# Kernel optimization log

Hardware: AMD Instinct MI355X
Metric: run time of the kernel (lower is better)

The kernel has to match this reference:

```python
import jax, jax.numpy as jnp
import numpy as np

NUM_HEADS = 16
NUM_GROUPS = 4
EPS = 1e-6


def _rope_tables(seq_len, head_dim):
    inv_freq = 1.0 / (10000.0 ** (jnp.arange(0, head_dim, 2, dtype=jnp.float32) / head_dim))
    t = jnp.arange(seq_len, dtype=jnp.float32)
    freqs = jnp.outer(t, inv_freq)  # [s, hd//2]
    return jnp.sin(freqs), jnp.cos(freqs)


def _apply_rope(x, sin, cos):
    # x: [b, s, h, hd]; sin/cos: [s, hd//2] -> broadcast over batch and heads
    sin = sin[None, :, None, :]
    cos = cos[None, :, None, :]
    x1 = x[..., ::2]
    x2 = x[..., 1::2]
    out1 = x1 * cos - x2 * sin
    out2 = x1 * sin + x2 * cos
    return jnp.stack([out1, out2], axis=-1).reshape(x.shape).astype(x.dtype)


def _rmsnorm(x, scale):
    var = jnp.mean(jnp.square(x), axis=-1, keepdims=True)
    return x * jax.lax.rsqrt(var + EPS) * scale


def setup_inputs() -> dict:
    key = jax.random.key(0)
    b, s, d = 16, 512, 2048
    hd = d // NUM_HEADS
    g = NUM_GROUPS
    ks = jax.random.split(key, 9)
    std = 0.02
    return {
        "x": jax.random.normal(ks[0], (b, s, d), dtype=jnp.float32),
        "Wq": jax.random.normal(ks[1], (d, d), dtype=jnp.float32) * std,
        "bq": jnp.zeros((d,), dtype=jnp.float32),
        "Wk": jax.random.normal(ks[2], (d, g * hd), dtype=jnp.float32) * std,
        "bk": jnp.zeros((g * hd,), dtype=jnp.float32),
        "Wv": jax.random.normal(ks[3], (d, g * hd), dtype=jnp.float32) * std,
        "bv": jnp.zeros((g * hd,), dtype=jnp.float32),
        "Wo": jax.random.normal(ks[4], (d, d), dtype=jnp.float32) * std,
        "bo": jnp.zeros((d,), dtype=jnp.float32),
        "q_norm_scale": jnp.ones((hd,), dtype=jnp.float32),
        "k_norm_scale": jnp.ones((hd,), dtype=jnp.float32),
    }


def reference(x, Wq, bq, Wk, bk, Wv, bv, Wo, bo, q_norm_scale, k_norm_scale):
    b, s, d = x.shape
    H, G = NUM_HEADS, NUM_GROUPS
    hd = d // H
    P = H // G  # queries per kv group
    inv_sqrt_hd = hd ** (-0.5)

    q = (x @ Wq + bq).reshape(b, s, H, hd)
    k = (x @ Wk + bk).reshape(b, s, G, hd)
    v = (x @ Wv + bv).reshape(b, s, G, hd)

    q = _rmsnorm(q, q_norm_scale)
    k = _rmsnorm(k, k_norm_scale)

    sin, cos = _rope_tables(s, hd)
    q = _apply_rope(q, sin, cos) * inv_sqrt_hd  # module pre-scales q
    k = _apply_rope(k, sin, cos)

    # GQA attention with causal mask; dot_product_attention applies an
    # additional 1/sqrt(hd) scale on top of the module's pre-scaling.
    qg = q.reshape(b, s, G, P, hd)
    logits = jnp.einsum("bsgph,btgh->bgpst", qg, k) * inv_sqrt_hd
    causal = jnp.tril(jnp.ones((s, s), dtype=bool))
    logits = jnp.where(causal[None, None, None, :, :], logits, jnp.finfo(logits.dtype).min)
    attn = jax.nn.softmax(logits, axis=-1)
    out = jnp.einsum("bgpst,btgh->bsgph", attn, v).reshape(b, s, d)
    return out @ Wo + bo
```

## Files before the change

### kernel.cpp

```cpp
#include <hip/hip_runtime.h>
#include <stdint.h>

typedef __attribute__((ext_vector_type(4))) float floatx4;
typedef __attribute__((ext_vector_type(16))) float floatx16;
typedef __attribute__((ext_vector_type(8))) short short8;

#define BB 16
#define SS 512
#define DD 2048
#define HH_ 16
#define HD 128
#define GG 4
#define MM (BB*SS)
#define NQKV 3072

__device__ __forceinline__ unsigned short f2bf(float f){
  unsigned u = __builtin_bit_cast(unsigned, f);
  u += 0x7fffu + ((u >> 16) & 1u);
  return (unsigned short)(u >> 16);
}
__device__ __forceinline__ float bf2f_lo(unsigned d){
  return __builtin_bit_cast(float, d << 16);
}
__device__ __forceinline__ float bf2f_hi(unsigned d){
  return __builtin_bit_cast(float, d & 0xffff0000u);
}

__device__ __forceinline__ void async_copy16(const void* g, void* l){
  __builtin_amdgcn_global_load_lds((const __attribute__((address_space(1))) unsigned*)g,
                                   (__attribute__((address_space(3))) unsigned*)l,
                                   16, 0, 0);
}

#define PB_CVT   16384
#define PB_TRQ   (PB_CVT + 4096)
#define PB_TRK   (PB_TRQ + 1024)
#define PB_TRV   (PB_TRK + 1024)
#define PB_TRO   (PB_TRV + 4096)
#define PB_ALL   (PB_TRO + 12)

__global__ __launch_bounds__(256) void prep_kernel(
    const float* __restrict__ x,
    const float* __restrict__ Wq, const float* __restrict__ Wk,
    const float* __restrict__ Wv, const float* __restrict__ Wo,
    const float* __restrict__ bq, const float* __restrict__ bk,
    const float* __restrict__ bv,
    unsigned short* __restrict__ xb, unsigned short* __restrict__ WqkvT,
    unsigned short* __restrict__ WoT, float* __restrict__ bqkv)
{
  __shared__ float tile[32][33];
  const int bid = blockIdx.x, tid = threadIdx.x;

  if (bid < PB_CVT) {
    const int i = bid * 256 + tid;
    float4 f = ((const float4*)x)[i];
    ushort4 o;
    o.x = f2bf(f.x); o.y = f2bf(f.y); o.z = f2bf(f.z); o.w = f2bf(f.w);
    ((ushort4*)xb)[i] = o;
    return;
  }
  if (bid < PB_TRO) {
    const float* src; unsigned short* dst; int R, C, b2;
    if (bid < PB_TRQ)      { src = Wq; dst = WqkvT;                          R = 2048; C = 2048; b2 = bid - PB_CVT; }
    else if (bid < PB_TRK) { src = Wk; dst = WqkvT + (size_t)2048 * 2048;    R = 2048; C = 512;  b2 = bid - PB_TRQ; }
    else if (bid < PB_TRV) { src = Wv; dst = WqkvT + (size_t)2560 * 2048;    R = 2048; C = 512;  b2 = bid - PB_TRK; }
    else                   { src = Wo; dst = WoT;                            R = 2048; C = 2048; b2 = bid - PB_TRV; }
    const int nbx = C >> 5;
    const int c0 = (b2 % nbx) * 32, r0 = (b2 / nbx) * 32;
    const int tx = tid & 31, ty = tid >> 5;
    #pragma unroll
    for (int j = 0; j < 32; j += 8)
      tile[ty + j][tx] = src[(size_t)(r0 + ty + j) * C + (c0 + tx)];
    __syncthreads();
    #pragma unroll
    for (int j = 0; j < 32; j += 8)
      dst[(size_t)(c0 + ty + j) * R + (r0 + tx)] = f2bf(tile[tx][ty + j]);
    return;
  }
  {
    const int i = (bid - PB_TRO) * 256 + tid;
    if (i < NQKV)
      bqkv[i] = (i < 2048) ? bq[i] : (i < 2560 ? bk[i - 2048] : bv[i - 2560]);
  }
}

template<bool OUT_BF16>
__global__ __launch_bounds__(512, 2) void gemm256_kernel(
    const unsigned short* __restrict__ A,
    const unsigned short* __restrict__ Bt,
    void* __restrict__ Cout,
    const float* __restrict__ bias,
    int N, int K, int ldc)
{
  __shared__ unsigned short sA[4 * 128 * 64];
  __shared__ unsigned short sB[4 * 128 * 64];

  const int tid  = threadIdx.x;
  const int wave = tid >> 6, lane = tid & 63;
  const int wm = wave >> 2, wn = wave & 3;
  const int l15 = lane & 15, l7 = lane & 7, q4 = lane >> 4;

  const int nbn = N >> 8;
  const int cpx = gridDim.x >> 3;
  const int bid = (blockIdx.x & 7) * cpx + (blockIdx.x >> 3);
  const int m0 = (bid / nbn) * 256;
  const int n0 = (bid % nbn) * 256;

  const int rowOff = wave * 8 + (lane >> 3);
  const int glog   = l7 ^ ((lane >> 3) & 7);
  const unsigned short* gA = A  + (size_t)(m0 + rowOff) * K + glog * 8;
  const unsigned short* gB = Bt + (size_t)(n0 + rowOff) * K + glog * 8;

#define STAGE_A(j, tt) do { \
    unsigned short* d_ = &sA[(2 * ((tt) & 1) + (j)) * 8192 + wave * 512]; \
    const unsigned short* s_ = gA + (size_t)((j) * 128) * K + (tt) * 64; \
    async_copy16(s_, d_); \
    async_copy16(s_ + (size_t)64 * K, d_ + 4096); } while (0)
#define STAGE_B(j, tt) do { \
    unsigned short* d_ = &sB[(2 * ((tt) & 1) + (j)) * 8192 + wave * 512]; \
    const unsigned short* s_ = gB + (size_t)((j) * 128) * K + (tt) * 64; \
    async_copy16(s_, d_); \
    async_copy16(s_ + (size_t)64 * K, d_ + 4096); } while (0)
#define FENCE() asm volatile("" ::: "memory")
#define BAR()   do { FENCE(); __builtin_amdgcn_s_barrier(); FENCE(); } while (0)

  STAGE_B(0, 0); STAGE_B(1, 0); STAGE_A(0, 0); STAGE_A(1, 0);
  STAGE_B(0, 1); STAGE_B(1, 1); STAGE_A(0, 1); STAGE_A(1, 1);

  floatx16 zero16 = {0.f};
  floatx4 acc[8][4];
  #pragma unroll
  for (int i = 0; i < 8; ++i)
    #pragma unroll
    for (int j = 0; j < 4; ++j)
      acc[i][j] = (floatx4){0.f, 0.f, 0.f, 0.f};
  (void)zero16;

  asm volatile("s_waitcnt vmcnt(8)" ::: "memory");
  BAR();

  short8 aF[4][2], bF[4][2];
  const int NT = K >> 6;

  const unsigned short* pA = &sA[l15 * 64];
  const unsigned short* pB = &sB[((wn & 1) * 64 + l15) * 64];
  const int g0 = ((0 + q4) ^ l7) * 8;
  const int g1 = ((4 + q4) ^ l7) * 8;

#define LDA_(fa_, rb_, sa_) do { \
    aF[fa_][0] = *(const short8*)(pA + (sa_) * 8192 + ((rb_) + (fa_) * 16) * 64 + g0); \
    aF[fa_][1] = *(const short8*)(pA + (sa_) * 8192 + ((rb_) + (fa_) * 16) * 64 + g1); } while (0)
#define LDB_(fb_, sb_) do { \
    bF[fb_][0] = *(const short8*)(pB + (sb_) * 8192 + (fb_) * 16 * 64 + g0); \
    bF[fb_][1] = *(const short8*)(pB + (sb_) * 8192 + (fb_) * 16 * 64 + g1); } while (0)
#define MFMA_Q(fa0, fb0) \
    _Pragma("unroll") \
    for (int fa = 0; fa < 4; ++fa) { \
      _Pragma("unroll") \
      for (int fb = 0; fb < 2; ++fb) { \
        acc[(fa0)+fa][(fb0)+fb] = __builtin_amdgcn_mfma_f32_16x16x32_bf16(aF[fa][0], bF[(fb0)+fb][0], acc[(fa0)+fa][(fb0)+fb], 0, 0, 0); \
        acc[(fa0)+fa][(fb0)+fb] = __builtin_amdgcn_mfma_f32_16x16x32_bf16(aF[fa][1], bF[(fb0)+fb][1], acc[(fa0)+fa][(fb0)+fb], 0, 0, 0); \
      } \
    }

  #pragma unroll 1
  for (int t = 0; t < NT; ++t) {
    const int sa = 2 * (t & 1) + wm;
    const int sb = 2 * (t & 1) + (wn >> 1);
    LDB_(0, sb); LDB_(1, sb);
    LDA_(0, 0, sa); LDA_(1, 0, sa); LDA_(2, 0, sa); LDA_(3, 0, sa);
    __builtin_amdgcn_s_setprio(1);
    MFMA_Q(0, 0);
    __builtin_amdgcn_s_setprio(0);
    BAR();
    LDB_(2, sb); LDB_(3, sb);
    __builtin_amdgcn_s_setprio(1);
    MFMA_Q(0, 2);
    __builtin_amdgcn_s_setprio(0);
    BAR();
    LDA_(0, 64, sa); LDA_(1, 64, sa); LDA_(2, 64, sa); LDA_(3, 64, sa);
    if (t + 2 < NT) { STAGE_B(0, t + 2); STAGE_B(1, t + 2); }
    __builtin_amdgcn_s_setprio(1);
    MFMA_Q(4, 0);
    __builtin_amdgcn_s_setprio(0);
    BAR();
    if (t + 2 < NT) {
      STAGE_A(0, t + 2); STAGE_A(1, t + 2);
      asm volatile("s_waitcnt vmcnt(8)" ::: "memory");
    } else if (t + 1 < NT) {
      asm volatile("s_waitcnt vmcnt(0)" ::: "memory");
    }
    __builtin_amdgcn_s_setprio(1);
    MFMA_Q(4, 2);
    __builtin_amdgcn_s_setprio(0);
    BAR();
  }
#undef STAGE_A
#undef STAGE_B
#undef LDA_
#undef LDB_
#undef MFMA_Q
#undef FENCE
#undef BAR

  const int r4 = q4 * 4;
  #pragma unroll
  for (int fb = 0; fb < 4; ++fb) {
    const int col = n0 + wn * 64 + fb * 16 + l15;
    const float bval = bias[col];
    #pragma unroll
    for (int fa = 0; fa < 8; ++fa) {
      const size_t rowb = (size_t)(m0 + wm * 128 + fa * 16 + r4);
      #pragma unroll
      for (int r = 0; r < 4; ++r) {
        const float v = acc[fa][fb][r] + bval;
        if (OUT_BF16)
          ((unsigned short*)Cout)[(rowb + r) * ldc + col] = f2bf(v);
        else
          ((float*)Cout)[(rowb + r) * ldc + col] = v;
      }
    }
  }
}

__global__ __launch_bounds__(256) void norm_vtr_kernel(
    unsigned short* __restrict__ qkv,
    const float* __restrict__ qs, const float* __restrict__ ks,
    unsigned short* __restrict__ vt)
{
  __shared__ unsigned short tileV[32][34];
  const int bid = blockIdx.x, tid = threadIdx.x;

  if (bid < 40960) {
    const int wave = tid >> 6, lane = tid & 63;
    const int gw  = bid * 4 + wave;
    const int row = gw / 20;
    const int hh  = gw % 20;
    const bool isq = hh < 16;

    unsigned* p = (unsigned*)(qkv + (size_t)row * NQKV + hh * 128) + lane;
    unsigned d = *p;
    float x1 = bf2f_lo(d), x2 = bf2f_hi(d);

    float ss = x1 * x1 + x2 * x2;
    #pragma unroll
    for (int off = 32; off; off >>= 1) ss += __shfl_xor(ss, off, 64);
    const float r = rsqrtf(ss * (1.f / 128.f) + 1e-6f);

    const float2 sc = ((const float2*)(isq ? qs : ks))[lane];
    float n1 = x1 * r * sc.x;
    float n2 = x2 * r * sc.y;

    const float t = (float)(row & (SS - 1));
    const float freq = __expf((float)lane * (-2.f / 128.f) * 9.21034037197618f);
    float sn, cs;
    __sincosf(t * freq, &sn, &cs);
    float o1 = n1 * cs - n2 * sn;
    float o2 = n1 * sn + n2 * cs;
    if (isq) { o1 *= (1.f / 128.f); o2 *= (1.f / 128.f); }

    *p = (unsigned)f2bf(o1) | ((unsigned)f2bf(o2) << 16);
    return;
  }
  {
    const int b2 = bid - 40960;
    const int hd0 = (b2 & 3) * 32, t0 = ((b2 >> 2) & 15) * 32, bg = b2 >> 6;
    const int tx = tid & 31, ty = tid >> 5;
    const int b = bg >> 2, g = bg & 3;
    const unsigned short* src = qkv + (size_t)b * SS * NQKV + 2560 + g * HD;
    #pragma unroll
    for (int j = 0; j < 32; j += 8)
      tileV[ty + j][tx] = src[(size_t)(t0 + ty + j) * NQKV + hd0 + tx];
    __syncthreads();
    unsigned short* dst = vt + (size_t)bg * HD * SS;
    #pragma unroll
    for (int j = 0; j < 32; j += 8)
      dst[(size_t)(hd0 + ty + j) * SS + t0 + tx] = tileV[tx][ty + j];
  }
}

__global__ __launch_bounds__(256, 4) void fattn_kernel(
    const unsigned short* __restrict__ qkv,
    const unsigned short* __restrict__ vtb,
    unsigned short* __restrict__ aout)
{
  __shared__ unsigned short sK[64 * 128];
  __shared__ unsigned short sV[128 * 64];
  __shared__ unsigned short sP[4][16 * 64];

  const int lane = threadIdx.x & 63, wave = threadIdx.x >> 6;
  const int quad = lane >> 4, col = lane & 15;
  const int idx = blockIdx.x;
  const int qb = 7 - (idx >> 8);
  const int bh = idx & 255;
  const int b = bh >> 4, h = bh & 15, g = h >> 2;

  const int qrow = qb * 64 + wave * 16 + col;
  const unsigned short* qg = qkv + ((size_t)(b * SS + qrow)) * NQKV + h * HD + quad * 8;
  short8 qf[4];
  #pragma unroll
  for (int c = 0; c < 4; ++c) qf[c] = *(const short8*)(qg + c * 32);

  const unsigned short* kg = qkv + (size_t)b * SS * NQKV + 2048 + g * HD;
  const unsigned short* vg = vtb + ((size_t)(b * GG + g)) * HD * SS;

  floatx4 acc_o[8];
  #pragma unroll
  for (int i = 0; i < 8; ++i) acc_o[i] = (floatx4){0.f, 0.f, 0.f, 0.f};
  float m[4] = {-INFINITY, -INFINITY, -INFINITY, -INFINITY};
  float l[4] = {0.f, 0.f, 0.f, 0.f};

  for (int kt = 0; kt <= qb; ++kt) {
    const int t0 = kt * 64;
    #pragma unroll
    for (int c = 0; c < 4; ++c) {
      const int ci = c * 4 + wave;
      { const int r  = ci * 4 + (lane >> 4);
        const int gl = (lane & 15) ^ (r & 15);
        async_copy16(kg + (size_t)(t0 + r) * NQKV + gl * 8, &sK[ci * 512]); }
      { const int r  = ci * 8 + (lane >> 3);
        const int gl = (lane & 7) ^ (r & 7);
        async_copy16(vg + (size_t)r * SS + t0 + gl * 8, &sV[ci * 512]); }
    }
    __syncthreads();

    floatx4 sc[4];
    #pragma unroll
    for (int s = 0; s < 4; ++s) sc[s] = (floatx4){0.f, 0.f, 0.f, 0.f};
    #pragma unroll
    for (int s = 0; s < 4; ++s) {
      const int trow = s * 16 + col;
      #pragma unroll
      for (int c = 0; c < 4; ++c) {
        const int p = (c * 4 + quad) ^ (trow & 15);
        const short8 kf = *(const short8*)(&sK[trow * 128 + p * 8]);
        sc[s] = __builtin_amdgcn_mfma_f32_16x16x32_bf16(qf[c], kf, sc[s], 0, 0, 0);
      }
    }

    if (kt == qb) {
      #pragma unroll
      for (int s = 0; s < 4; ++s)
        #pragma unroll
        for (int r = 0; r < 4; ++r)
          if (s * 16 + col > wave * 16 + quad * 4 + r) sc[s][r] = -1e30f;
    }

    float mx[4], alpha[4], lsum[4];
    #pragma unroll
    for (int r = 0; r < 4; ++r) {
      mx[r] = fmaxf(fmaxf(sc[0][r], sc[1][r]), fmaxf(sc[2][r], sc[3][r]));
      #pragma unroll
      for (int off = 8; off; off >>= 1) mx[r] = fmaxf(mx[r], __shfl_xor(mx[r], off, 16));
      mx[r] = fmaxf(mx[r], m[r]);
      alpha[r] = __expf(m[r] - mx[r]);
      m[r] = mx[r];
      lsum[r] = 0.f;
    }
    #pragma unroll
    for (int s = 0; s < 4; ++s)
      #pragma unroll
      for (int r = 0; r < 4; ++r) {
        const float p = __expf(sc[s][r] - m[r]);
        lsum[r] += p;
        const int row = quad * 4 + r;
        const int slot = (s * 2 + (col >> 3)) ^ (row & 7);
        sP[wave][row * 64 + slot * 8 + (col & 7)] = f2bf(p);
      }
    #pragma unroll
    for (int r = 0; r < 4; ++r) {
      #pragma unroll
      for (int off = 8; off; off >>= 1) lsum[r] += __shfl_xor(lsum[r], off, 16);
      l[r] = l[r] * alpha[r] + lsum[r];
    }
    #pragma unroll
    for (int n = 0; n < 8; ++n)
      #pragma unroll
      for (int r = 0; r < 4; ++r) acc_o[n][r] *= alpha[r];

    __asm__ volatile("s_waitcnt lgkmcnt(0)" ::: "memory");

    short8 pf[2];
    #pragma unroll
    for (int kc = 0; kc < 2; ++kc)
      pf[kc] = *(const short8*)(&sP[wave][col * 64 + ((kc * 4 + quad) ^ (col & 7)) * 8]);
    #pragma unroll
    for (int n = 0; n < 8; ++n) {
      const int hdrow = n * 16 + col;
      #pragma unroll
      for (int kc = 0; kc < 2; ++kc) {
        const int p = (kc * 4 + quad) ^ (hdrow & 7);
        const short8 vf = *(const short8*)(&sV[hdrow * 64 + p * 8]);
        acc_o[n] = __builtin_amdgcn_mfma_f32_16x16x32_bf16(pf[kc], vf, acc_o[n], 0, 0, 0);
      }
    }
    __syncthreads();
  }

  float inv[4];
  #pragma unroll
  for (int r = 0; r < 4; ++r) inv[r] = 1.f / l[r];
  unsigned short* ob = aout + ((size_t)(b * SS + qb * 64 + wave * 16)) * DD + h * HD;
  #pragma unroll
  for (int n = 0; n < 8; ++n)
    #pragma unroll
    for (int r = 0; r < 4; ++r)
      ob[(size_t)(quad * 4 + r) * DD + n * 16 + col] = f2bf(acc_o[n][r] * inv[r]);
}

extern "C" void kernel_launch(void* const* d_in, const int* in_sizes, int n_in,
                              void* d_out, int out_size, void* d_ws, size_t ws_size,
                              hipStream_t stream) {
  const float* x   = (const float*)d_in[0];
  const float* Wq  = (const float*)d_in[1];
  const float* bq  = (const float*)d_in[2];
  const float* Wk  = (const float*)d_in[3];
  const float* bk  = (const float*)d_in[4];
  const float* Wv  = (const float*)d_in[5];
  const float* bv  = (const float*)d_in[6];
  const float* Wo  = (const float*)d_in[7];
  const float* bo  = (const float*)d_in[8];
  const float* qns = (const float*)d_in[9];
  const float* kns = (const float*)d_in[10];

  char* ws = (char*)d_ws;
  unsigned short* xb    = (unsigned short*)(ws);
  unsigned short* vtb   = (unsigned short*)(ws);
  unsigned short* WqkvT = (unsigned short*)(ws + 33554432);
  unsigned short* WoT   = (unsigned short*)(ws + 46137344);
  float*          bqkv  = (float*)         (ws + 54525952);
  unsigned short* qkv   = (unsigned short*)(ws + 54538240);
  unsigned short* aout  = (unsigned short*)(ws + 104869888);

  prep_kernel<<<PB_ALL, 256, 0, stream>>>(x, Wq, Wk, Wv, Wo, bq, bk, bv,
                                          xb, WqkvT, WoT, bqkv);
  gemm256_kernel<true><<<384, 512, 0, stream>>>(xb, WqkvT, qkv, bqkv,
                                                NQKV, DD, NQKV);
  norm_vtr_kernel<<<45056, 256, 0, stream>>>(qkv, qns, kns, vtb);
  fattn_kernel<<<2048, 256, 0, stream>>>(qkv, vtb, aout);
  gemm256_kernel<false><<<256, 512, 0, stream>>>(aout, WoT, d_out, bo,
                                                 DD, DD, DD);
  (void)in_sizes; (void)n_in; (void)out_size; (void)ws_size;
}
```

Baseline: 426.0 us.

## Double-buffer attention K/V tiles and swap QKV GEMM to simpler 128x128 kernel

```diff
diff --git a/kernel.cpp b/kernel.cpp
--- a/kernel.cpp
+++ b/kernel.cpp
@@ -81,6 +81,86 @@
     const int i = (bid - PB_TRO) * 256 + tid;
     if (i < NQKV)
       bqkv[i] = (i < 2048) ? bq[i] : (i < 2560 ? bk[i - 2048] : bv[i - 2560]);
+  }
+}
+
+template<bool OUT_BF16>
+__global__ __launch_bounds__(256) void gemm_bt_kernel(
+    const unsigned short* __restrict__ A,
+    const unsigned short* __restrict__ Bt,
+    void* __restrict__ Cout,
+    const float* __restrict__ bias,
+    int M, int N, int K, int ldc)
+{
+  __shared__ unsigned short sA[128 * 64];
+  __shared__ unsigned short sB[128 * 64];
+  const int tid  = threadIdx.x;
+  const int wave = tid >> 6;
+  const int lane = tid & 63;
+  const int m0 = blockIdx.y * 128;
+  const int n0 = blockIdx.x * 128;
+  const int wm = (wave >> 1) * 64;
+  const int wn = (wave & 1) * 64;
+
+  floatx16 acc[2][2];
+  #pragma unroll
+  for (int i = 0; i < 2; i++)
+    #pragma unroll
+    for (int j = 0; j < 2; j++)
+      #pragma unroll
+      for (int r = 0; r < 16; r++) acc[i][j][r] = 0.f;
+
+  const int sglog = (lane & 7) ^ ((lane >> 3) & 7);
+  const unsigned short* gA = A  + (size_t)(m0 + 32 * wave + (lane >> 3)) * K + sglog * 8;
+  const unsigned short* gB = Bt + (size_t)(n0 + 32 * wave + (lane >> 3)) * K + sglog * 8;
+  unsigned short* lA = &sA[32 * wave * 64];
+  unsigned short* lB = &sB[32 * wave * 64];
+
+  for (int k0 = 0; k0 < K; k0 += 64) {
+    #pragma unroll
+    for (int c = 0; c < 4; ++c) {
+      async_copy16(gA + (size_t)c * 8 * K + k0, lA + c * 512);
+      async_copy16(gB + (size_t)c * 8 * K + k0, lB + c * 512);
+    }
+    __syncthreads();
+
+    #pragma unroll
+    for (int kh = 0; kh < 4; ++kh) {
+      const int slot = (kh * 2 + (lane >> 5)) ^ (lane & 7);
+      short8 aF[2], bF[2];
+      #pragma unroll
+      for (int i = 0; i < 2; ++i)
+        aF[i] = *(const short8*)(&sA[(wm + i * 32 + (lane & 31)) * 64 + slot * 8]);
+      #pragma unroll
+      for (int j = 0; j < 2; ++j)
+        bF[j] = *(const short8*)(&sB[(wn + j * 32 + (lane & 31)) * 64 + slot * 8]);
+      #pragma unroll
+      for (int i = 0; i < 2; ++i)
+        #pragma unroll
+        for (int j = 0; j < 2; ++j)
+          acc[i][j] = __builtin_amdgcn_mfma_f32_32x32x16_bf16(aF[i], bF[j], acc[i][j], 0, 0, 0);
+    }
+    __syncthreads();
+  }
+
+  const int cc = lane & 31;
+  const int rb = 4 * (lane >> 5);
+  #pragma unroll
+  for (int j = 0; j < 2; j++) {
+    const int col = n0 + wn + j * 32 + cc;
+    const float bval = bias[col];
+    #pragma unroll
+    for (int i = 0; i < 2; i++) {
+      #pragma unroll
+      for (int reg = 0; reg < 16; reg++) {
+        const int row = m0 + wm + i * 32 + (reg & 3) + 8 * (reg >> 2) + rb;
+        const float v = acc[i][j][reg] + bval;
+        if (OUT_BF16)
+          ((unsigned short*)Cout)[(size_t)row * ldc + col] = f2bf(v);
+        else
+          ((float*)Cout)[(size_t)row * ldc + col] = v;
+      }
+    }
   }
 }
 
@@ -127,14 +207,12 @@
   STAGE_B(0, 0); STAGE_B(1, 0); STAGE_A(0, 0); STAGE_A(1, 0);
   STAGE_B(0, 1); STAGE_B(1, 1); STAGE_A(0, 1); STAGE_A(1, 1);
 
-  floatx16 zero16 = {0.f};
   floatx4 acc[8][4];
   #pragma unroll
   for (int i = 0; i < 8; ++i)
     #pragma unroll
     for (int j = 0; j < 4; ++j)
       acc[i][j] = (floatx4){0.f, 0.f, 0.f, 0.f};
-  (void)zero16;
 
   asm volatile("s_waitcnt vmcnt(8)" ::: "memory");
   BAR();
@@ -279,13 +357,13 @@
   }
 }
 
-__global__ __launch_bounds__(256, 4) void fattn_kernel(
+__global__ __launch_bounds__(256, 2) void fattn_kernel(
     const unsigned short* __restrict__ qkv,
     const unsigned short* __restrict__ vtb,
     unsigned short* __restrict__ aout)
 {
-  __shared__ unsigned short sK[64 * 128];
-  __shared__ unsigned short sV[128 * 64];
+  __shared__ unsigned short sK[2][64 * 128];
+  __shared__ unsigned short sV[2][128 * 64];
   __shared__ unsigned short sP[4][16 * 64];
 
   const int lane = threadIdx.x & 63, wave = threadIdx.x >> 6;
@@ -310,33 +388,41 @@
   float m[4] = {-INFINITY, -INFINITY, -INFINITY, -INFINITY};
   float l[4] = {0.f, 0.f, 0.f, 0.f};
 
+#define STAGE_KV(kt_, bf_) do { \
+    const int t0_ = (kt_) * 64; \
+    _Pragma("unroll") \
+    for (int c = 0; c < 4; ++c) { \
+      const int ci = c * 4 + wave; \
+      { const int r_  = ci * 4 + (lane >> 4); \
+        const int gl_ = (lane & 15) ^ (r_ & 15); \
+        async_copy16(kg + (size_t)(t0_ + r_) * NQKV + gl_ * 8, &sK[bf_][ci * 512]); } \
+      { const int r_  = ci * 8 + (lane >> 3); \
+        const int gl_ = (lane & 7) ^ (r_ & 7); \
+        async_copy16(vg + (size_t)r_ * SS + t0_ + gl_ * 8, &sV[bf_][ci * 512]); } \
+    } } while (0)
+
+  STAGE_KV(0, 0);
+
   for (int kt = 0; kt <= qb; ++kt) {
-    const int t0 = kt * 64;
-    #pragma unroll
-    for (int c = 0; c < 4; ++c) {
-      const int ci = c * 4 + wave;
-      { const int r  = ci * 4 + (lane >> 4);
-        const int gl = (lane & 15) ^ (r & 15);
-        async_copy16(kg + (size_t)(t0 + r) * NQKV + gl * 8, &sK[ci * 512]); }
-      { const int r  = ci * 8 + (lane >> 3);
-        const int gl = (lane & 7) ^ (r & 7);
-        async_copy16(vg + (size_t)r * SS + t0 + gl * 8, &sV[ci * 512]); }
-    }
+    const int buf = kt & 1;
     __syncthreads();
+    if (kt < qb) STAGE_KV(kt + 1, buf ^ 1);
 
     floatx4 sc[4];
     #pragma unroll
     for (int s = 0; s < 4; ++s) sc[s] = (floatx4){0.f, 0.f, 0.f, 0.f};
+    __builtin_amdgcn_s_setprio(1);
     #pragma unroll
     for (int s = 0; s < 4; ++s) {
       const int trow = s * 16 + col;
       #pragma unroll
       for (int c = 0; c < 4; ++c) {
         const int p = (c * 4 + quad) ^ (trow & 15);
-        const short8 kf = *(const short8*)(&sK[trow * 128 + p * 8]);
+        const short8 kf = *(const short8*)(&sK[buf][trow * 128 + p * 8]);
         sc[s] = __builtin_amdgcn_mfma_f32_16x16x32_bf16(qf[c], kf, sc[s], 0, 0, 0);
       }
     }
+    __builtin_amdgcn_s_setprio(0);
 
     if (kt == qb) {
       #pragma unroll
@@ -378,24 +464,24 @@
       #pragma unroll
       for (int r = 0; r < 4; ++r) acc_o[n][r] *= alpha[r];
 
-    __asm__ volatile("s_waitcnt lgkmcnt(0)" ::: "memory");
-
     short8 pf[2];
     #pragma unroll
     for (int kc = 0; kc < 2; ++kc)
       pf[kc] = *(const short8*)(&sP[wave][col * 64 + ((kc * 4 + quad) ^ (col & 7)) * 8]);
+    __builtin_amdgcn_s_setprio(1);
     #pragma unroll
     for (int n = 0; n < 8; ++n) {
       const int hdrow = n * 16 + col;
       #pragma unroll
       for (int kc = 0; kc < 2; ++kc) {
         const int p = (kc * 4 + quad) ^ (hdrow & 7);
-        const short8 vf = *(const short8*)(&sV[hdrow * 64 + p * 8]);
+        const short8 vf = *(const short8*)(&sV[buf][hdrow * 64 + p * 8]);
         acc_o[n] = __builtin_amdgcn_mfma_f32_16x16x32_bf16(pf[kc], vf, acc_o[n], 0, 0, 0);
       }
     }
-    __syncthreads();
-  }
+    __builtin_amdgcn_s_setprio(0);
+  }
+#undef STAGE_KV
 
   float inv[4];
   #pragma unroll
@@ -434,8 +520,8 @@
 
   prep_kernel<<<PB_ALL, 256, 0, stream>>>(x, Wq, Wk, Wv, Wo, bq, bk, bv,
                                           xb, WqkvT, WoT, bqkv);
-  gemm256_kernel<true><<<384, 512, 0, stream>>>(xb, WqkvT, qkv, bqkv,
-                                                NQKV, DD, NQKV);
+  gemm_bt_kernel<true><<<dim3(24, 64), 256, 0, stream>>>(xb, WqkvT, qkv, bqkv,
+                                                         MM, NQKV, DD, NQKV);
   norm_vtr_kernel<<<45056, 256, 0, stream>>>(qkv, qns, kns, vtb);
   fattn_kernel<<<2048, 256, 0, stream>>>(qkv, vtb, aout);
   gemm256_kernel<false><<<256, 512, 0, stream>>>(aout, WoT, d_out, bo,
```

New measurement: 420.4 us. No clear change (-1.3%).
